# Optimization experiments

Measured on AMD Instinct MI355X. Metric: run time of the kernel, lower is better.

## Reference

```python
import jax, jax.numpy as jnp
import numpy as np
from jax.scipy.special import logsumexp

TEMPERATURE = 0.05
HARD_NEG_WEIGHT = 1.0
MARGIN = 0.2
EXPLICIT_NEG_WEIGHT = 2.0
NEG_INF = -1e9


def setup_inputs() -> dict:
    key = jax.random.key(0)
    k1, k2, k3 = jax.random.split(key, 3)
    N, D = 8192, 512
    return {
        "asm_embeddings": jax.random.normal(k1, (N, D), dtype=jnp.float32),
        "source_embeddings": jax.random.normal(k2, (N, D), dtype=jnp.float32),
        "labels": jax.random.randint(k3, (N,), 0, 2, dtype=jnp.int64),
    }


def reference(asm_embeddings, source_embeddings, labels):
    # L2-normalize both embedding sets
    a = asm_embeddings / jnp.linalg.norm(asm_embeddings, axis=1, keepdims=True)
    s = source_embeddings / jnp.linalg.norm(source_embeddings, axis=1, keepdims=True)
    sim = jnp.matmul(a, s.T) / TEMPERATURE  # [N, N]

    N = labels.shape[0]
    pos_mask = labels == 1
    neg_mask = labels == 0
    num_pos = jnp.sum(pos_mask).astype(sim.dtype)
    num_neg = jnp.sum(neg_mask)

    # column weights: explicit negatives (label==0) get EXPLICIT_NEG_WEIGHT,
    # others 1; the positive (diagonal) logit always has weight 1.
    log_w = jnp.log(jnp.where(neg_mask, EXPLICIT_NEG_WEIGHT, 1.0).astype(sim.dtype))
    eye = jnp.eye(N, dtype=bool)
    weighted_logits = sim + jnp.where(eye, 0.0, log_w[None, :])  # [N, N]

    lse = logsumexp(weighted_logits, axis=1)  # weighted logsumexp per row
    diag = jnp.diagonal(sim)
    per_row_loss = lse - diag  # -log_prob_pos

    infonce = jnp.sum(jnp.where(pos_mask, per_row_loss, 0.0)) / num_pos

    # margin penalty on hardest explicit-negative diagonal similarity
    mean_pos_sim = jnp.sum(jnp.where(pos_mask, diag, 0.0)) / num_pos
    hard_neg_sim = jnp.max(jnp.where(neg_mask, diag, NEG_INF))
    penalty = jax.nn.relu(hard_neg_sim - mean_pos_sim + MARGIN)
    penalty = jnp.where(num_neg > 0, penalty, 0.0)

    return infonce + HARD_NEG_WEIGHT * penalty
```

## Files before the change

kernel.cpp:

```cpp
#include <hip/hip_runtime.h>
#include <math.h>

#define NROWS 8192
#define DIM 512
#define INV_T 20.0f
#define QS 500.0f
#define DEQ2 (INV_T * 1.4426950408889634f / (QS * QS))

typedef __attribute__((ext_vector_type(4))) int i32x4;

__device__ __forceinline__ void gload_lds16(const void* g, void* l) {
    __builtin_amdgcn_global_load_lds(
        (const __attribute__((address_space(1))) unsigned int*)g,
        (__attribute__((address_space(3))) unsigned int*)l, 16, 0, 0);
}

__device__ __forceinline__ float hw_exp2(float x) {
    float r;
    asm("v_exp_f32 %0, %1" : "=v"(r) : "v"(x));
    return r;
}

__device__ __forceinline__ float dot4(float4 a, float4 b) {
    return a.x * b.x + a.y * b.y + a.z * b.z + a.w * b.w;
}

__device__ __forceinline__ int q4(float4 v, float s) {
    int b0 = __float2int_rn(fminf(fmaxf(v.x * s, -127.f), 127.f)) & 255;
    int b1 = __float2int_rn(fminf(fmaxf(v.y * s, -127.f), 127.f)) & 255;
    int b2 = __float2int_rn(fminf(fmaxf(v.z * s, -127.f), 127.f)) & 255;
    int b3 = __float2int_rn(fminf(fmaxf(v.w * s, -127.f), 127.f)) & 255;
    return b0 | (b1 << 8) | (b2 << 16) | (b3 << 24);
}

__global__ __launch_bounds__(256) void norm_kernel(
    const float* __restrict__ A, const float* __restrict__ S,
    const int* __restrict__ labels, signed char* __restrict__ aQ,
    signed char* __restrict__ sQ, float* __restrict__ diag,
    float* __restrict__ lw2, float* __restrict__ lsum) {
    const int wave = threadIdx.x >> 6, lane = threadIdx.x & 63;
    const int row = blockIdx.x * 4 + wave;
    const float4* a4 = (const float4*)(A + (size_t)row * DIM);
    const float4* s4 = (const float4*)(S + (size_t)row * DIM);
    float4 a0 = a4[lane], a1 = a4[lane + 64];
    float4 s0 = s4[lane], s1 = s4[lane + 64];
    float saa = dot4(a0, a0) + dot4(a1, a1);
    float sss = dot4(s0, s0) + dot4(s1, s1);
    float sas = dot4(a0, s0) + dot4(a1, s1);
    for (int m = 1; m < 64; m <<= 1) {
        saa += __shfl_xor(saa, m);
        sss += __shfl_xor(sss, m);
        sas += __shfl_xor(sas, m);
    }
    const float ra = rsqrtf(saa), rs = rsqrtf(sss);
    signed char* arow = aQ + (size_t)row * DIM;
    signed char* srow = sQ + (size_t)row * DIM;
    *(int*)(arow + lane * 4)       = q4(a0, ra * QS);
    *(int*)(arow + 256 + lane * 4) = q4(a1, ra * QS);
    *(int*)(srow + lane * 4)       = q4(s0, rs * QS);
    *(int*)(srow + 256 + lane * 4) = q4(s1, rs * QS);
    if (lane == 0) {
        diag[row] = sas * ra * rs * INV_T;
        lw2[row] = (labels[row] == 0) ? 1.0f : 0.0f;
        lsum[row] = 0.0f;
    }
}

__global__ __launch_bounds__(1024) void lse_gemm(
    const signed char* __restrict__ Aq, const signed char* __restrict__ Bq,
    const float* __restrict__ lw2, float* __restrict__ lsum) {
    __shared__ __align__(16) char lds[65536];

    const int bid = blockIdx.x;
    const int xcd = bid & 7, idx = bid >> 3;
    const int rt = (xcd >> 1) * 8 + (idx & 7);
    const int ctg = (xcd & 1) * 4 + (idx >> 3);
    const int row0 = rt * 256;
    const int colg = ctg * 1024;

    const int tid = threadIdx.x;
    const int wid = tid >> 6, lane = tid & 63;
    const int wr = wid >> 2, wc = wid & 3;
    const int fr = lane & 15, grp = lane >> 4;

    const int srow = tid >> 2;
    const int sl = (tid & 3) ^ ((tid >> 3) & 3);
    const signed char* aSrc = Aq + (size_t)(row0 + srow) * DIM + sl * 16;
    const signed char* bSrc = Bq + (size_t)(colg + srow) * DIM + sl * 16;
    char* dstA = lds + tid * 16;
    char* dstB = lds + 16384 + tid * 16;

#define STAGE(buf, TT)                                                        \
    do {                                                                      \
        const int ct_ = (TT) >> 3, k_ = (TT) & 7;                             \
        gload_lds16(aSrc + k_ * 64, dstA + (buf) * 32768);                    \
        gload_lds16(bSrc + ct_ * 131072 + k_ * 64, dstB + (buf) * 32768);     \
    } while (0)

    const int ps = (grp ^ ((fr >> 1) & 3)) << 4;
    const char* rdA = lds + (wr * 64 + fr) * 64 + ps;
    const char* rdB = lds + 16384 + (wc * 64 + fr) * 64 + ps;

    STAGE(0, 0);

    i32x4 acc[4][4] = {};
#pragma unroll 2
    for (int T = 0; T < 32; ++T) {
        const int buf = T & 1;
        if (T < 31) {
            STAGE(buf ^ 1, T + 1);
            asm volatile("s_waitcnt vmcnt(2)" ::: "memory");
        } else {
            asm volatile("s_waitcnt vmcnt(0)" ::: "memory");
        }
        __builtin_amdgcn_s_barrier();

        i32x4 a[4], b[4];
#pragma unroll
        for (int m = 0; m < 4; ++m)
            a[m] = *(const i32x4*)(rdA + buf * 32768 + m * 1024);
#pragma unroll
        for (int n = 0; n < 4; ++n)
            b[n] = *(const i32x4*)(rdB + buf * 32768 + n * 1024);
        asm volatile("s_waitcnt lgkmcnt(0)" ::: "memory");
        __builtin_amdgcn_sched_barrier(0);

        __builtin_amdgcn_s_setprio(1);
#pragma unroll
        for (int m = 0; m < 4; ++m)
#pragma unroll
            for (int n = 0; n < 4; ++n)
                acc[m][n] = __builtin_amdgcn_mfma_i32_16x16x64_i8(
                    a[m], b[n], acc[m][n], 0, 0, 0);
        __builtin_amdgcn_s_setprio(0);

        if ((T & 7) == 7) {
            const int ct = T >> 3;
            const int col0 = colg + ct * 256 + wc * 64;
            float lwv[4];
#pragma unroll
            for (int n = 0; n < 4; ++n)
                lwv[n] = lw2[col0 + n * 16 + fr];
#pragma unroll
            for (int m = 0; m < 4; ++m)
#pragma unroll
                for (int j = 0; j < 4; ++j) {
                    float s = 0.f;
#pragma unroll
                    for (int n = 0; n < 4; ++n)
                        s += hw_exp2(fmaf((float)acc[m][n][j], DEQ2, lwv[n]));
                    s += __shfl_xor(s, 1);
                    s += __shfl_xor(s, 2);
                    s += __shfl_xor(s, 4);
                    s += __shfl_xor(s, 8);
                    if (fr == 0)
                        atomicAdd(&lsum[row0 + wr * 64 + m * 16 + grp * 4 + j], s);
                }
#pragma unroll
            for (int m = 0; m < 4; ++m)
#pragma unroll
                for (int n = 0; n < 4; ++n)
                    acc[m][n] = i32x4{0, 0, 0, 0};
        }
        __builtin_amdgcn_s_barrier();
    }
#undef STAGE
}

__global__ __launch_bounds__(1024) void finalize_kernel(
    const float* __restrict__ lsum, const float* __restrict__ diag,
    const int* __restrict__ labels, float* __restrict__ out) {
    const int tid = threadIdx.x;
    float sl = 0.f, sd = 0.f, mx = -1e9f;
    int np_ = 0, nn_ = 0;
#pragma unroll
    for (int i = tid; i < NROWS; i += 1024) {
        const float dg = diag[i];
        if (labels[i] == 1) {
            sl += logf(lsum[i]) - dg;
            sd += dg;
            np_++;
        } else {
            nn_++;
            mx = fmaxf(mx, dg);
        }
    }
    for (int m = 1; m < 64; m <<= 1) {
        sl += __shfl_xor(sl, m);
        sd += __shfl_xor(sd, m);
        mx = fmaxf(mx, __shfl_xor(mx, m));
        np_ += __shfl_xor(np_, m);
        nn_ += __shfl_xor(nn_, m);
    }
    __shared__ float rsl[16], rsd[16], rmx[16];
    __shared__ int rnp[16], rnn[16];
    const int wave = tid >> 6, lane = tid & 63;
    if (lane == 0) {
        rsl[wave] = sl; rsd[wave] = sd; rmx[wave] = mx;
        rnp[wave] = np_; rnn[wave] = nn_;
    }
    __syncthreads();
    if (tid == 0) {
        float SL = 0.f, SD = 0.f, MX = -1e9f;
        int NP = 0, NN = 0;
        for (int w = 0; w < 16; w++) {
            SL += rsl[w]; SD += rsd[w]; MX = fmaxf(MX, rmx[w]);
            NP += rnp[w]; NN += rnn[w];
        }
        const float infonce = SL / (float)NP;
        const float meanpos = SD / (float)NP;
        float pen = fmaxf(MX - meanpos + 0.2f, 0.0f);
        if (NN == 0) pen = 0.0f;
        out[0] = infonce + pen;
    }
}

extern "C" void kernel_launch(void* const* d_in, const int* in_sizes, int n_in,
                              void* d_out, int out_size, void* d_ws, size_t ws_size,
                              hipStream_t stream) {
    const float* A = (const float*)d_in[0];
    const float* S = (const float*)d_in[1];
    const int* labels = (const int*)d_in[2];
    float* out = (float*)d_out;

    char* ws = (char*)d_ws;
    signed char* aQ = (signed char*)ws;
    signed char* sQ = (signed char*)(ws + (size_t)NROWS * DIM);
    char* p = ws + (size_t)NROWS * DIM * 2;
    float* diag = (float*)p;
    float* lw2 = (float*)(p + 32768);
    float* lsum = (float*)(p + 65536);

    norm_kernel<<<NROWS / 4, 256, 0, stream>>>(A, S, labels, aQ, sQ, diag, lw2, lsum);
    lse_gemm<<<256, 1024, 0, stream>>>(aQ, sQ, lw2, lsum);
    finalize_kernel<<<1, 1024, 0, stream>>>(lsum, diag, labels, out);
}
```

Baseline: 65.77 us.

## Double K-step per stage in int8 LSE GEMM to halve barriers

Each pipeline stage of the int8 GEMM now loads a 128-byte K slice per row instead of 64, with a wider XOR swizzle, so the loop runs 16 iterations instead of 32. Each iteration performs two MFMA sub-steps. The goal is to halve the per-iteration barrier and waitcnt overhead and issue larger global-to-LDS batches. In exchange the kernel uses 128 KB of LDS, which limits occupancy to one 1024-thread block per CU, and there are more in-flight loads per stage.

Measured after the change: 65.05 us. Within noise of the previous version (-1.1%).

```diff
diff --git a/kernel.cpp b/kernel.cpp
--- a/kernel.cpp
+++ b/kernel.cpp
@@ -13,6 +13,12 @@
     __builtin_amdgcn_global_load_lds(
         (const __attribute__((address_space(1))) unsigned int*)g,
         (__attribute__((address_space(3))) unsigned int*)l, 16, 0, 0);
+}
+
+__device__ __forceinline__ void block_bar() {
+    asm volatile("" ::: "memory");
+    __builtin_amdgcn_s_barrier();
+    asm volatile("" ::: "memory");
 }
 
 __device__ __forceinline__ float hw_exp2(float x) {
@@ -66,10 +72,10 @@
     }
 }
 
-__global__ __launch_bounds__(1024) void lse_gemm(
+__global__ __launch_bounds__(1024, 4) void lse_gemm(
     const signed char* __restrict__ Aq, const signed char* __restrict__ Bq,
     const float* __restrict__ lw2, float* __restrict__ lsum) {
-    __shared__ __align__(16) char lds[65536];
+    __shared__ __align__(16) char lds[131072];
 
     const int bid = blockIdx.x;
     const int xcd = bid & 7, idx = bid >> 3;
@@ -82,60 +88,66 @@
     const int wid = tid >> 6, lane = tid & 63;
     const int wr = wid >> 2, wc = wid & 3;
     const int fr = lane & 15, grp = lane >> 4;
-
-    const int srow = tid >> 2;
-    const int sl = (tid & 3) ^ ((tid >> 3) & 3);
-    const signed char* aSrc = Aq + (size_t)(row0 + srow) * DIM + sl * 16;
-    const signed char* bSrc = Bq + (size_t)(colg + srow) * DIM + sl * 16;
+    const int f7 = fr & 7;
+
+    const int sl = (tid & 7) ^ ((tid >> 3) & 7);
+    const signed char* aSrc = Aq + (size_t)(row0 + (tid >> 3)) * DIM + sl * 16;
+    const signed char* bSrc = Bq + (size_t)(colg + (tid >> 3)) * DIM + sl * 16;
     char* dstA = lds + tid * 16;
-    char* dstB = lds + 16384 + tid * 16;
+    char* dstB = lds + 32768 + tid * 16;
 
 #define STAGE(buf, TT)                                                        \
     do {                                                                      \
-        const int ct_ = (TT) >> 3, k_ = (TT) & 7;                             \
-        gload_lds16(aSrc + k_ * 64, dstA + (buf) * 32768);                    \
-        gload_lds16(bSrc + ct_ * 131072 + k_ * 64, dstB + (buf) * 32768);     \
+        const int ct_ = (TT) >> 2, k_ = (TT) & 3;                             \
+        gload_lds16(aSrc + k_ * 128,                     dstA + (buf) * 65536); \
+        gload_lds16(aSrc + 65536 + k_ * 128,             dstA + (buf) * 65536 + 16384); \
+        gload_lds16(bSrc + ct_ * 131072 + k_ * 128,      dstB + (buf) * 65536); \
+        gload_lds16(bSrc + ct_ * 131072 + 65536 + k_ * 128, dstB + (buf) * 65536 + 16384); \
     } while (0)
 
-    const int ps = (grp ^ ((fr >> 1) & 3)) << 4;
-    const char* rdA = lds + (wr * 64 + fr) * 64 + ps;
-    const char* rdB = lds + 16384 + (wc * 64 + fr) * 64 + ps;
+    const char* rdA = lds + (wr * 64 + fr) * 128;
+    const char* rdB = lds + 32768 + (wc * 64 + fr) * 128;
 
     STAGE(0, 0);
 
     i32x4 acc[4][4] = {};
-#pragma unroll 2
-    for (int T = 0; T < 32; ++T) {
+#pragma unroll 1
+    for (int T = 0; T < 16; ++T) {
         const int buf = T & 1;
-        if (T < 31) {
+        if (T < 15) {
             STAGE(buf ^ 1, T + 1);
-            asm volatile("s_waitcnt vmcnt(2)" ::: "memory");
+            asm volatile("s_waitcnt vmcnt(4)" ::: "memory");
         } else {
             asm volatile("s_waitcnt vmcnt(0)" ::: "memory");
         }
-        __builtin_amdgcn_s_barrier();
-
-        i32x4 a[4], b[4];
-#pragma unroll
-        for (int m = 0; m < 4; ++m)
-            a[m] = *(const i32x4*)(rdA + buf * 32768 + m * 1024);
-#pragma unroll
-        for (int n = 0; n < 4; ++n)
-            b[n] = *(const i32x4*)(rdB + buf * 32768 + n * 1024);
-        asm volatile("s_waitcnt lgkmcnt(0)" ::: "memory");
-        __builtin_amdgcn_sched_barrier(0);
-
-        __builtin_amdgcn_s_setprio(1);
-#pragma unroll
-        for (int m = 0; m < 4; ++m)
+        block_bar();
+
+        const char* bA = rdA + buf * 65536;
+        const char* bB = rdB + buf * 65536;
+#pragma unroll
+        for (int ks = 0; ks < 2; ++ks) {
+            const int psk = ((ks * 4 + grp) ^ f7) << 4;
+            i32x4 a[4], b[4];
+#pragma unroll
+            for (int m = 0; m < 4; ++m)
+                a[m] = *(const i32x4*)(bA + m * 2048 + psk);
 #pragma unroll
             for (int n = 0; n < 4; ++n)
-                acc[m][n] = __builtin_amdgcn_mfma_i32_16x16x64_i8(
-                    a[m], b[n], acc[m][n], 0, 0, 0);
-        __builtin_amdgcn_s_setprio(0);
-
-        if ((T & 7) == 7) {
-            const int ct = T >> 3;
+                b[n] = *(const i32x4*)(bB + n * 2048 + psk);
+            asm volatile("s_waitcnt lgkmcnt(0)" ::: "memory");
+            __builtin_amdgcn_sched_barrier(0);
+            __builtin_amdgcn_s_setprio(1);
+#pragma unroll
+            for (int m = 0; m < 4; ++m)
+#pragma unroll
+                for (int n = 0; n < 4; ++n)
+                    acc[m][n] = __builtin_amdgcn_mfma_i32_16x16x64_i8(
+                        a[m], b[n], acc[m][n], 0, 0, 0);
+            __builtin_amdgcn_s_setprio(0);
+        }
+
+        if ((T & 3) == 3) {
+            const int ct = T >> 2;
             const int col0 = colg + ct * 256 + wc * 64;
             float lwv[4];
 #pragma unroll
@@ -162,7 +174,7 @@
                 for (int n = 0; n < 4; ++n)
                     acc[m][n] = i32x4{0, 0, 0, 0};
         }
-        __builtin_amdgcn_s_barrier();
+        block_bar();
     }
 #undef STAGE
 }
```
